# Kernel optimization log

Measured on AMD Instinct MI355X. Metric: run time of the kernel, lower is better.

## Reference

```python
import jax, jax.numpy as jnp
import numpy as np

N_GOAL, N_OBS, N_TASK = 16384, 65536, 8192
E1, E2 = 1048576, 1048576
B = 256            # graphs in batch
F, S = 128, 64     # dim_features, dim_state


def setup_inputs() -> dict:
    key = jax.random.key(0)
    ks = jax.random.split(key, 16)
    inp = {
        "x_goal": jax.random.normal(ks[0], (N_GOAL, F), jnp.float32),
        "x_obs": jax.random.normal(ks[1], (N_OBS, F), jnp.float32),
        "x_task": jax.random.normal(ks[2], (N_TASK, S), jnp.float32),
        "ei_go_src": jax.random.randint(ks[3], (E1,), 0, N_GOAL),
        "ei_go_dst": jax.random.randint(ks[4], (E1,), 0, N_OBS),
        "ei_ot_src": jax.random.randint(ks[5], (E2,), 0, N_OBS),
        "ei_ot_dst": jax.random.randint(ks[6], (E2,), 0, N_TASK),
        # contiguous graph assignment: 32 task nodes per graph
        "task_batch": jnp.arange(N_TASK) // (N_TASK // B),
        # GinStandardMLP (state_gin): Lin(F,S)-ReLU-Lin(S,S)-ReLU
        "W1": jax.random.normal(ks[7], (F, S), jnp.float32) * 0.05,
        "b1": jnp.zeros((S,), jnp.float32),
        "W2": jax.random.normal(ks[8], (S, S), jnp.float32) * 0.05,
        "b2": jnp.zeros((S,), jnp.float32),
        # GinUnactivatedMLP (action_gin): Lin(S,S)-ReLU-Lin(S,1)
        "W3": jax.random.normal(ks[9], (S, S), jnp.float32) * 0.05,
        "b3": jnp.zeros((S,), jnp.float32),
        "W4": jax.random.normal(ks[10], (S, 1), jnp.float32) * 0.05,
        "b4": jnp.zeros((1,), jnp.float32),
        # critic head: Lin(2,8)-ReLU-Lin(8,1)
        "Wc1": jax.random.normal(ks[11], (2, 8), jnp.float32) * 0.5,
        "bc1": jnp.zeros((8,), jnp.float32),
        "Wc2": jax.random.normal(ks[12], (8, 1), jnp.float32) * 0.5,
        "bc2": jnp.zeros((1,), jnp.float32),
    }
    return inp


def reference(x_goal, x_obs, x_task,
              ei_go_src, ei_go_dst, ei_ot_src, ei_ot_dst, task_batch,
              W1, b1, W2, b2, W3, b3, W4, b4, Wc1, bc1, Wc2, bc2):
    # --- state_gin: GINConv((goal, obs)), eps=0 ---
    agg1 = jax.ops.segment_sum(x_goal[ei_go_src], ei_go_dst, num_segments=N_OBS)
    h = x_obs + agg1                              # (1+eps)*x_dst + sum_j x_src
    h = jax.nn.relu(h @ W1 + b1)
    x1 = jax.nn.relu(h @ W2 + b2)                 # [N_OBS, S]

    # --- action_gin: GINConv((obs, task)), eps=0 ---
    agg2 = jax.ops.segment_sum(x1[ei_ot_src], ei_ot_dst, num_segments=N_TASK)
    g = x_task + agg2
    g = jax.nn.relu(g @ W3 + b3)
    x2 = g @ W4 + b4                              # [N_TASK, 1]

    # --- critic path: global max / mean pool over task nodes per graph ---
    max_pool = jax.ops.segment_max(x2, task_batch, num_segments=B)   # [B, 1]
    cnt = jax.ops.segment_sum(jnp.ones((N_TASK, 1), x2.dtype), task_batch, num_segments=B)
    mean_pool = jax.ops.segment_sum(x2, task_batch, num_segments=B) / cnt  # [B, 1]

    pooled = jnp.concatenate([max_pool.max(axis=1, keepdims=True),
                              mean_pool.mean(axis=1, keepdims=True)], axis=1)  # [B, 2]
    out = jax.nn.relu(pooled @ Wc1 + bc1) @ Wc2 + bc2                 # [B, 1]
    return out.squeeze(-1)                                            # [B]
```

## Files before the change

kernel.cpp:

```cpp
#include <hip/hip_runtime.h>
#include <hip/hip_bf16.h>


#define NB 512
#define BUCKET_CAP 2816

__global__ __launch_bounds__(256) void gemm_k128(
    const float* __restrict__ X, const float* __restrict__ W,
    float* __restrict__ out, int M)
{
    __shared__ float Ws[128 * 64];
    __shared__ float Xs[16 * 132];
    const int tid = threadIdx.x;
    for (int i = tid; i < 128 * 64 / 4; i += 256)
        ((float4*)Ws)[i] = ((const float4*)W)[i];
    const int row0 = blockIdx.x * 16;
    for (int i = tid; i < 16 * 32; i += 256) {
        int r = i >> 5, c4 = i & 31;
        float4 v = ((const float4*)(X + (size_t)(row0 + r) * 128))[c4];
        *((float4*)(Xs + r * 132 + c4 * 4)) = v;
    }
    __syncthreads();
    const int rl = tid >> 4;
    const int cg = (tid & 15) * 4;
    float a0 = 0.f, a1 = 0.f, a2 = 0.f, a3 = 0.f;
    const float* xr = Xs + rl * 132;
    #pragma unroll 8
    for (int k = 0; k < 128; ++k) {
        float xv = xr[k];
        float4 wv = *((const float4*)(Ws + k * 64 + cg));
        a0 = fmaf(xv, wv.x, a0);
        a1 = fmaf(xv, wv.y, a1);
        a2 = fmaf(xv, wv.z, a2);
        a3 = fmaf(xv, wv.w, a3);
    }
    float4 o; o.x = a0; o.y = a1; o.z = a2; o.w = a3;
    *((float4*)(out + (size_t)(row0 + rl) * 64 + cg)) = o;
}

template <int BSH>
__global__ __launch_bounds__(256) void bin_edges(
    const int* __restrict__ src, const int* __restrict__ dst,
    int* __restrict__ gcur, int2* __restrict__ pairs)
{
    __shared__ int hist[NB];
    __shared__ int cur[NB];
    const int tid = threadIdx.x;
    for (int i = tid; i < NB; i += 256) hist[i] = 0;
    __syncthreads();
    const int base = blockIdx.x * 4096;
    const int4* d4 = (const int4*)(dst + base);
    const int4* s4 = (const int4*)(src + base);
    int4 dv[4];
    #pragma unroll
    for (int k = 0; k < 4; ++k) {
        dv[k] = d4[k * 256 + tid];
        atomicAdd(&hist[dv[k].x >> BSH], 1);
        atomicAdd(&hist[dv[k].y >> BSH], 1);
        atomicAdd(&hist[dv[k].z >> BSH], 1);
        atomicAdd(&hist[dv[k].w >> BSH], 1);
    }
    __syncthreads();
    for (int i = tid; i < NB; i += 256)
        cur[i] = atomicAdd(&gcur[i], hist[i]);
    __syncthreads();
    #pragma unroll
    for (int k = 0; k < 4; ++k) {
        int4 sv = s4[k * 256 + tid];
        int d, s, b, p;
        d = dv[k].x; s = sv.x; b = d >> BSH; p = atomicAdd(&cur[b], 1);
        if (p < BUCKET_CAP) pairs[(size_t)b * BUCKET_CAP + p] = make_int2(d, s);
        d = dv[k].y; s = sv.y; b = d >> BSH; p = atomicAdd(&cur[b], 1);
        if (p < BUCKET_CAP) pairs[(size_t)b * BUCKET_CAP + p] = make_int2(d, s);
        d = dv[k].z; s = sv.z; b = d >> BSH; p = atomicAdd(&cur[b], 1);
        if (p < BUCKET_CAP) pairs[(size_t)b * BUCKET_CAP + p] = make_int2(d, s);
        d = dv[k].w; s = sv.w; b = d >> BSH; p = atomicAdd(&cur[b], 1);
        if (p < BUCKET_CAP) pairs[(size_t)b * BUCKET_CAP + p] = make_int2(d, s);
    }
}

template <int BSH, bool ADD_BASE>
__global__ __launch_bounds__(1024) void gather_sorted(
    const int2* __restrict__ pairs, const int* __restrict__ cnt,
    const float* __restrict__ table, float* __restrict__ outb)
{
    constexpr int ROWS = 1 << BSH;
    constexpr int ROWM = ROWS - 1;
    __shared__ int ssrc[BUCKET_CAP];
    __shared__ int offs[ROWS + 1];
    __shared__ int cur[ROWS];
    __shared__ int sc[ROWS];
    const int tid = threadIdx.x;
    const int b = blockIdx.x;

    for (int i = tid; i < ROWS; i += 1024) cur[i] = 0;
    __syncthreads();
    int n = cnt[b];
    if (n > BUCKET_CAP) n = BUCKET_CAP;
    const int2* bp = pairs + (size_t)b * BUCKET_CAP;

    for (int i = tid; i < n; i += 1024)
        atomicAdd(&cur[bp[i].x & ROWM], 1);
    __syncthreads();
    if (tid < ROWS) sc[tid] = cur[tid];
    __syncthreads();
    for (int off = 1; off < ROWS; off <<= 1) {
        int v = 0;
        if (tid < ROWS && tid >= off) v = sc[tid - off];
        __syncthreads();
        if (tid < ROWS) sc[tid] += v;
        __syncthreads();
    }
    if (tid < ROWS) {
        int ex = (tid == 0) ? 0 : sc[tid - 1];
        offs[tid] = ex;
        cur[tid] = ex;
        if (tid == ROWS - 1) offs[ROWS] = sc[tid];
    }
    __syncthreads();
    for (int i = tid; i < n; i += 1024) {
        int2 p = bp[i];
        int pos = atomicAdd(&cur[p.x & ROWM], 1);
        ssrc[pos] = p.y;
    }
    __syncthreads();
    const int wv = tid >> 6;
    const int lane = tid & 63;
    for (int r = wv; r < ROWS; r += 16) {
        int beg = offs[r], end = offs[r + 1];
        float a0 = 0.f, a1 = 0.f, a2 = 0.f, a3 = 0.f;
        int e = beg;
        for (; e + 4 <= end; e += 4) {
            int s0 = ssrc[e], s1 = ssrc[e + 1], s2 = ssrc[e + 2], s3 = ssrc[e + 3];
            a0 += table[(size_t)s0 * 64 + lane];
            a1 += table[(size_t)s1 * 64 + lane];
            a2 += table[(size_t)s2 * 64 + lane];
            a3 += table[(size_t)s3 * 64 + lane];
        }
        for (; e < end; ++e)
            a0 += table[(size_t)ssrc[e] * 64 + lane];
        float acc = (a0 + a1) + (a2 + a3);
        size_t gi = (((size_t)b << BSH) + r) * 64 + lane;
        if (ADD_BASE) acc += outb[gi];
        outb[gi] = acc;
    }
}

__global__ __launch_bounds__(256) void mlp_obs(
    const float* __restrict__ in, const float* __restrict__ b1,
    const float* __restrict__ W2, const float* __restrict__ b2,
    float* __restrict__ out, int M)
{
    __shared__ float Ws[64 * 64];
    __shared__ float Hs[16 * 68];
    const int tid = threadIdx.x;
    for (int i = tid; i < 64 * 64 / 4; i += 256)
        ((float4*)Ws)[i] = ((const float4*)W2)[i];
    const int row0 = blockIdx.x * 16;
    {
        int r = tid >> 4, c4 = tid & 15;
        float4 v = ((const float4*)(in + (size_t)(row0 + r) * 64))[c4];
        float4 bb = ((const float4*)b1)[c4];
        v.x = fmaxf(v.x + bb.x, 0.f);
        v.y = fmaxf(v.y + bb.y, 0.f);
        v.z = fmaxf(v.z + bb.z, 0.f);
        v.w = fmaxf(v.w + bb.w, 0.f);
        *((float4*)(Hs + r * 68 + c4 * 4)) = v;
    }
    __syncthreads();
    const int rl = tid >> 4, cg = (tid & 15) * 4;
    float4 bb2 = *((const float4*)(b2 + cg));
    float a0 = bb2.x, a1 = bb2.y, a2 = bb2.z, a3 = bb2.w;
    const float* hr = Hs + rl * 68;
    #pragma unroll 8
    for (int k = 0; k < 64; ++k) {
        float xv = hr[k];
        float4 wv = *((const float4*)(Ws + k * 64 + cg));
        a0 = fmaf(xv, wv.x, a0);
        a1 = fmaf(xv, wv.y, a1);
        a2 = fmaf(xv, wv.z, a2);
        a3 = fmaf(xv, wv.w, a3);
    }
    float4 o;
    o.x = fmaxf(a0, 0.f); o.y = fmaxf(a1, 0.f);
    o.z = fmaxf(a2, 0.f); o.w = fmaxf(a3, 0.f);
    *((float4*)(out + (size_t)(row0 + rl) * 64 + cg)) = o;
}

__global__ __launch_bounds__(512) void mlp_task_pool(
    const float* __restrict__ x_task, const float* __restrict__ acc2,
    const float* __restrict__ W3, const float* __restrict__ b3,
    const float* __restrict__ W4, const float* __restrict__ b4,
    const float* __restrict__ Wc1, const float* __restrict__ bc1,
    const float* __restrict__ Wc2, const float* __restrict__ bc2,
    float* __restrict__ out)
{
    __shared__ float Ws[64 * 64];
    __shared__ float Ts[32 * 68];
    __shared__ float xrow[32];
    const int tid = threadIdx.x;
    for (int i = tid; i < 64 * 64 / 4; i += 512)
        ((float4*)Ws)[i] = ((const float4*)W3)[i];
    const int row0 = blockIdx.x * 32;
    {
        int r = tid >> 4, c4 = tid & 15;
        size_t off = (size_t)(row0 + r) * 64;
        float4 v = ((const float4*)(x_task + off))[c4];
        float4 u = ((const float4*)(acc2 + off))[c4];
        v.x += u.x; v.y += u.y; v.z += u.z; v.w += u.w;
        *((float4*)(Ts + r * 68 + c4 * 4)) = v;
    }
    __syncthreads();
    const int rl = tid >> 4, cg = (tid & 15) * 4;
    float4 bb = *((const float4*)(b3 + cg));
    float a0 = bb.x, a1 = bb.y, a2 = bb.z, a3 = bb.w;
    const float* tr = Ts + rl * 68;
    #pragma unroll 8
    for (int k = 0; k < 64; ++k) {
        float xv = tr[k];
        float4 wv = *((const float4*)(Ws + k * 64 + cg));
        a0 = fmaf(xv, wv.x, a0);
        a1 = fmaf(xv, wv.y, a1);
        a2 = fmaf(xv, wv.z, a2);
        a3 = fmaf(xv, wv.w, a3);
    }
    float4 w4 = *((const float4*)(W4 + cg));
    float p = fmaxf(a0, 0.f) * w4.x + fmaxf(a1, 0.f) * w4.y
            + fmaxf(a2, 0.f) * w4.z + fmaxf(a3, 0.f) * w4.w;
    p += __shfl_xor(p, 1);
    p += __shfl_xor(p, 2);
    p += __shfl_xor(p, 4);
    p += __shfl_xor(p, 8);
    if ((tid & 15) == 0) xrow[rl] = p + b4[0];
    __syncthreads();
    if (tid == 0) {
        float mx = -1e30f, sm = 0.f;
        #pragma unroll
        for (int i = 0; i < 32; ++i) { float v = xrow[i]; mx = fmaxf(mx, v); sm += v; }
        float mn = sm * (1.f / 32.f);
        float o = bc2[0];
        #pragma unroll
        for (int j = 0; j < 8; ++j) {
            float t = fmaxf(mx * Wc1[j] + mn * Wc1[8 + j] + bc1[j], 0.f);
            o = fmaf(t, Wc2[j], o);
        }
        out[blockIdx.x] = o;
    }
}

extern "C" void kernel_launch(void* const* d_in, const int* in_sizes, int n_in,
                              void* d_out, int out_size, void* d_ws, size_t ws_size,
                              hipStream_t stream)
{
    const float* x_goal = (const float*)d_in[0];
    const float* x_obs  = (const float*)d_in[1];
    const float* x_task = (const float*)d_in[2];
    const int* go_src = (const int*)d_in[3];
    const int* go_dst = (const int*)d_in[4];
    const int* ot_src = (const int*)d_in[5];
    const int* ot_dst = (const int*)d_in[6];
    const float* W1  = (const float*)d_in[8];
    const float* b1  = (const float*)d_in[9];
    const float* W2  = (const float*)d_in[10];
    const float* b2  = (const float*)d_in[11];
    const float* W3  = (const float*)d_in[12];
    const float* b3  = (const float*)d_in[13];
    const float* W4  = (const float*)d_in[14];
    const float* b4  = (const float*)d_in[15];
    const float* Wc1 = (const float*)d_in[16];
    const float* bc1 = (const float*)d_in[17];
    const float* Wc2 = (const float*)d_in[18];
    const float* bc2 = (const float*)d_in[19];
    float* out = (float*)d_out;

    const int N_GOAL = 16384, N_OBS = 65536, N_TASK = 8192;
    const int E1 = in_sizes[3], E2 = in_sizes[5];

    char* w = (char*)d_ws;
    float* obs   = (float*)w;   w += (size_t)N_OBS * 64 * 4;
    float* xg1   = (float*)w;   w += (size_t)N_GOAL * 64 * 4;
    float* acc2  = (float*)w;   w += (size_t)N_TASK * 64 * 4;
    int2*  pairs = (int2*)w;    w += (size_t)NB * BUCKET_CAP * 8;
    int*   gcur1 = (int*)w;     w += NB * 4;
    int*   gcur2 = (int*)w;     w += NB * 4;

    hipMemsetAsync(gcur1, 0, 2 * NB * 4, stream);

    bin_edges<7><<<E1 / 4096, 256, 0, stream>>>(go_src, go_dst, gcur1, pairs);
    gemm_k128<<<N_GOAL / 16, 256, 0, stream>>>(x_goal, W1, xg1, N_GOAL);
    gemm_k128<<<N_OBS / 16, 256, 0, stream>>>(x_obs, W1, obs, N_OBS);
    gather_sorted<7, true><<<NB, 1024, 0, stream>>>(pairs, gcur1, xg1, obs);
    mlp_obs<<<N_OBS / 16, 256, 0, stream>>>(obs, b1, W2, b2, obs, N_OBS);

    bin_edges<4><<<E2 / 4096, 256, 0, stream>>>(ot_src, ot_dst, gcur2, pairs);
    gather_sorted<4, false><<<NB, 1024, 0, stream>>>(pairs, gcur2, obs, acc2);
    mlp_task_pool<<<N_TASK / 32, 512, 0, stream>>>(x_task, acc2, W3, b3, W4, b4,
                                                   Wc1, bc1, Wc2, bc2, out);
}
```

Measured before the change: 270.7 us.

## Fuse gathers with MLP layers and pack edge pairs into single ints

Edge pairs are packed into one 32-bit int (local row in the high bits, source index in the low 17 bits), which halves bucket traffic. The obs gather is fused with bias, ReLU and the W2 layer, and the task gather is fused with the W3 and W4 layers. This removes the separate mlp_obs and mlp_task_pool passes and their intermediate round trips through global memory. Pooling moves to a tiny single-block kernel, and the second binning now runs early into its own buffer. The fused per-wave 64x64 matvec from shared memory may use compute less efficiently than the old tiled GEMM.

```diff
diff --git a/kernel.cpp b/kernel.cpp
--- a/kernel.cpp
+++ b/kernel.cpp
@@ -41,8 +41,9 @@
 template <int BSH>
 __global__ __launch_bounds__(256) void bin_edges(
     const int* __restrict__ src, const int* __restrict__ dst,
-    int* __restrict__ gcur, int2* __restrict__ pairs)
-{
+    int* __restrict__ gcur, int* __restrict__ pairs)
+{
+    constexpr int ROWM = (1 << BSH) - 1;
     __shared__ int hist[NB];
     __shared__ int cur[NB];
     const int tid = threadIdx.x;
@@ -69,38 +70,41 @@
         int4 sv = s4[k * 256 + tid];
         int d, s, b, p;
         d = dv[k].x; s = sv.x; b = d >> BSH; p = atomicAdd(&cur[b], 1);
-        if (p < BUCKET_CAP) pairs[(size_t)b * BUCKET_CAP + p] = make_int2(d, s);
+        if (p < BUCKET_CAP) pairs[(size_t)b * BUCKET_CAP + p] = ((d & ROWM) << 17) | s;
         d = dv[k].y; s = sv.y; b = d >> BSH; p = atomicAdd(&cur[b], 1);
-        if (p < BUCKET_CAP) pairs[(size_t)b * BUCKET_CAP + p] = make_int2(d, s);
+        if (p < BUCKET_CAP) pairs[(size_t)b * BUCKET_CAP + p] = ((d & ROWM) << 17) | s;
         d = dv[k].z; s = sv.z; b = d >> BSH; p = atomicAdd(&cur[b], 1);
-        if (p < BUCKET_CAP) pairs[(size_t)b * BUCKET_CAP + p] = make_int2(d, s);
+        if (p < BUCKET_CAP) pairs[(size_t)b * BUCKET_CAP + p] = ((d & ROWM) << 17) | s;
         d = dv[k].w; s = sv.w; b = d >> BSH; p = atomicAdd(&cur[b], 1);
-        if (p < BUCKET_CAP) pairs[(size_t)b * BUCKET_CAP + p] = make_int2(d, s);
-    }
-}
-
-template <int BSH, bool ADD_BASE>
-__global__ __launch_bounds__(1024) void gather_sorted(
-    const int2* __restrict__ pairs, const int* __restrict__ cnt,
-    const float* __restrict__ table, float* __restrict__ outb)
-{
-    constexpr int ROWS = 1 << BSH;
-    constexpr int ROWM = ROWS - 1;
+        if (p < BUCKET_CAP) pairs[(size_t)b * BUCKET_CAP + p] = ((d & ROWM) << 17) | s;
+    }
+}
+
+__global__ __launch_bounds__(1024) void gather_mlp_obs(
+    const int* __restrict__ pairs, const int* __restrict__ cnt,
+    const float* __restrict__ xg1, const float* __restrict__ obs,
+    const float* __restrict__ b1, const float* __restrict__ W2,
+    const float* __restrict__ b2, float* __restrict__ x1)
+{
+    constexpr int ROWS = 128;
     __shared__ int ssrc[BUCKET_CAP];
     __shared__ int offs[ROWS + 1];
     __shared__ int cur[ROWS];
     __shared__ int sc[ROWS];
+    __shared__ float W2s[64 * 64];
+    __shared__ float hb[16 * 64];
     const int tid = threadIdx.x;
     const int b = blockIdx.x;
 
-    for (int i = tid; i < ROWS; i += 1024) cur[i] = 0;
+    ((float4*)W2s)[tid] = ((const float4*)W2)[tid];
+    if (tid < ROWS) cur[tid] = 0;
     __syncthreads();
     int n = cnt[b];
     if (n > BUCKET_CAP) n = BUCKET_CAP;
-    const int2* bp = pairs + (size_t)b * BUCKET_CAP;
+    const int* bp = pairs + (size_t)b * BUCKET_CAP;
 
     for (int i = tid; i < n; i += 1024)
-        atomicAdd(&cur[bp[i].x & ROWM], 1);
+        atomicAdd(&cur[bp[i] >> 17], 1);
     __syncthreads();
     if (tid < ROWS) sc[tid] = cur[tid];
     __syncthreads();
@@ -119,133 +123,149 @@
     }
     __syncthreads();
     for (int i = tid; i < n; i += 1024) {
-        int2 p = bp[i];
-        int pos = atomicAdd(&cur[p.x & ROWM], 1);
-        ssrc[pos] = p.y;
+        int p = bp[i];
+        int pos = atomicAdd(&cur[p >> 17], 1);
+        ssrc[pos] = p & 0x1FFFF;
     }
     __syncthreads();
     const int wv = tid >> 6;
     const int lane = tid & 63;
+    const float bb1 = b1[lane];
+    const float bb2 = b2[lane];
+    float* hp = hb + wv * 64;
     for (int r = wv; r < ROWS; r += 16) {
         int beg = offs[r], end = offs[r + 1];
         float a0 = 0.f, a1 = 0.f, a2 = 0.f, a3 = 0.f;
         int e = beg;
         for (; e + 4 <= end; e += 4) {
             int s0 = ssrc[e], s1 = ssrc[e + 1], s2 = ssrc[e + 2], s3 = ssrc[e + 3];
-            a0 += table[(size_t)s0 * 64 + lane];
-            a1 += table[(size_t)s1 * 64 + lane];
-            a2 += table[(size_t)s2 * 64 + lane];
-            a3 += table[(size_t)s3 * 64 + lane];
+            a0 += xg1[(size_t)s0 * 64 + lane];
+            a1 += xg1[(size_t)s1 * 64 + lane];
+            a2 += xg1[(size_t)s2 * 64 + lane];
+            a3 += xg1[(size_t)s3 * 64 + lane];
         }
         for (; e < end; ++e)
-            a0 += table[(size_t)ssrc[e] * 64 + lane];
-        float acc = (a0 + a1) + (a2 + a3);
-        size_t gi = (((size_t)b << BSH) + r) * 64 + lane;
-        if (ADD_BASE) acc += outb[gi];
-        outb[gi] = acc;
-    }
-}
-
-__global__ __launch_bounds__(256) void mlp_obs(
-    const float* __restrict__ in, const float* __restrict__ b1,
-    const float* __restrict__ W2, const float* __restrict__ b2,
-    float* __restrict__ out, int M)
-{
-    __shared__ float Ws[64 * 64];
-    __shared__ float Hs[16 * 68];
-    const int tid = threadIdx.x;
-    for (int i = tid; i < 64 * 64 / 4; i += 256)
-        ((float4*)Ws)[i] = ((const float4*)W2)[i];
-    const int row0 = blockIdx.x * 16;
-    {
-        int r = tid >> 4, c4 = tid & 15;
-        float4 v = ((const float4*)(in + (size_t)(row0 + r) * 64))[c4];
-        float4 bb = ((const float4*)b1)[c4];
-        v.x = fmaxf(v.x + bb.x, 0.f);
-        v.y = fmaxf(v.y + bb.y, 0.f);
-        v.z = fmaxf(v.z + bb.z, 0.f);
-        v.w = fmaxf(v.w + bb.w, 0.f);
-        *((float4*)(Hs + r * 68 + c4 * 4)) = v;
-    }
-    __syncthreads();
-    const int rl = tid >> 4, cg = (tid & 15) * 4;
-    float4 bb2 = *((const float4*)(b2 + cg));
-    float a0 = bb2.x, a1 = bb2.y, a2 = bb2.z, a3 = bb2.w;
-    const float* hr = Hs + rl * 68;
-    #pragma unroll 8
-    for (int k = 0; k < 64; ++k) {
-        float xv = hr[k];
-        float4 wv = *((const float4*)(Ws + k * 64 + cg));
-        a0 = fmaf(xv, wv.x, a0);
-        a1 = fmaf(xv, wv.y, a1);
-        a2 = fmaf(xv, wv.z, a2);
-        a3 = fmaf(xv, wv.w, a3);
-    }
-    float4 o;
-    o.x = fmaxf(a0, 0.f); o.y = fmaxf(a1, 0.f);
-    o.z = fmaxf(a2, 0.f); o.w = fmaxf(a3, 0.f);
-    *((float4*)(out + (size_t)(row0 + rl) * 64 + cg)) = o;
-}
-
-__global__ __launch_bounds__(512) void mlp_task_pool(
-    const float* __restrict__ x_task, const float* __restrict__ acc2,
+            a0 += xg1[(size_t)ssrc[e] * 64 + lane];
+        size_t gi = (((size_t)b * ROWS) + r) * 64 + lane;
+        float acc = (a0 + a1) + (a2 + a3) + obs[gi];
+        hp[lane] = fmaxf(acc + bb1, 0.f);
+        float a = bb2;
+        #pragma unroll 16
+        for (int k = 0; k < 64; ++k)
+            a = fmaf(hp[k], W2s[k * 64 + lane], a);
+        x1[gi] = fmaxf(a, 0.f);
+    }
+}
+
+__global__ __launch_bounds__(1024) void gather_mlp_task(
+    const int* __restrict__ pairs, const int* __restrict__ cnt,
+    const float* __restrict__ x1, const float* __restrict__ x_task,
     const float* __restrict__ W3, const float* __restrict__ b3,
     const float* __restrict__ W4, const float* __restrict__ b4,
-    const float* __restrict__ Wc1, const float* __restrict__ bc1,
-    const float* __restrict__ Wc2, const float* __restrict__ bc2,
-    float* __restrict__ out)
-{
-    __shared__ float Ws[64 * 64];
-    __shared__ float Ts[32 * 68];
-    __shared__ float xrow[32];
+    float* __restrict__ x2)
+{
+    constexpr int ROWS = 16;
+    __shared__ int ssrc[BUCKET_CAP];
+    __shared__ int offs[ROWS + 1];
+    __shared__ int cur[ROWS];
+    __shared__ int sc[ROWS];
+    __shared__ float W3s[64 * 64];
+    __shared__ float hb[16 * 64];
     const int tid = threadIdx.x;
-    for (int i = tid; i < 64 * 64 / 4; i += 512)
-        ((float4*)Ws)[i] = ((const float4*)W3)[i];
-    const int row0 = blockIdx.x * 32;
-    {
-        int r = tid >> 4, c4 = tid & 15;
-        size_t off = (size_t)(row0 + r) * 64;
-        float4 v = ((const float4*)(x_task + off))[c4];
-        float4 u = ((const float4*)(acc2 + off))[c4];
-        v.x += u.x; v.y += u.y; v.z += u.z; v.w += u.w;
-        *((float4*)(Ts + r * 68 + c4 * 4)) = v;
-    }
-    __syncthreads();
-    const int rl = tid >> 4, cg = (tid & 15) * 4;
-    float4 bb = *((const float4*)(b3 + cg));
-    float a0 = bb.x, a1 = bb.y, a2 = bb.z, a3 = bb.w;
-    const float* tr = Ts + rl * 68;
-    #pragma unroll 8
-    for (int k = 0; k < 64; ++k) {
-        float xv = tr[k];
-        float4 wv = *((const float4*)(Ws + k * 64 + cg));
-        a0 = fmaf(xv, wv.x, a0);
-        a1 = fmaf(xv, wv.y, a1);
-        a2 = fmaf(xv, wv.z, a2);
-        a3 = fmaf(xv, wv.w, a3);
-    }
-    float4 w4 = *((const float4*)(W4 + cg));
-    float p = fmaxf(a0, 0.f) * w4.x + fmaxf(a1, 0.f) * w4.y
-            + fmaxf(a2, 0.f) * w4.z + fmaxf(a3, 0.f) * w4.w;
+    const int b = blockIdx.x;
+
+    ((float4*)W3s)[tid] = ((const float4*)W3)[tid];
+    if (tid < ROWS) cur[tid] = 0;
+    __syncthreads();
+    int n = cnt[b];
+    if (n > BUCKET_CAP) n = BUCKET_CAP;
+    const int* bp = pairs + (size_t)b * BUCKET_CAP;
+
+    for (int i = tid; i < n; i += 1024)
+        atomicAdd(&cur[bp[i] >> 17], 1);
+    __syncthreads();
+    if (tid < ROWS) sc[tid] = cur[tid];
+    __syncthreads();
+    for (int off = 1; off < ROWS; off <<= 1) {
+        int v = 0;
+        if (tid < ROWS && tid >= off) v = sc[tid - off];
+        __syncthreads();
+        if (tid < ROWS) sc[tid] += v;
+        __syncthreads();
+    }
+    if (tid < ROWS) {
+        int ex = (tid == 0) ? 0 : sc[tid - 1];
+        offs[tid] = ex;
+        cur[tid] = ex;
+        if (tid == ROWS - 1) offs[ROWS] = sc[tid];
+    }
+    __syncthreads();
+    for (int i = tid; i < n; i += 1024) {
+        int p = bp[i];
+        int pos = atomicAdd(&cur[p >> 17], 1);
+        ssrc[pos] = p & 0x1FFFF;
+    }
+    __syncthreads();
+
+    const int wv = tid >> 6;
+    const int lane = tid & 63;
+    const int r = wv;
+    const int row = b * ROWS + r;
+    int beg = offs[r], end = offs[r + 1];
+    float a0 = 0.f, a1 = 0.f, a2 = 0.f, a3 = 0.f;
+    float a4 = 0.f, a5 = 0.f, a6 = 0.f, a7 = 0.f;
+    int e = beg;
+    for (; e + 8 <= end; e += 8) {
+        int s0 = ssrc[e],     s1 = ssrc[e + 1], s2 = ssrc[e + 2], s3 = ssrc[e + 3];
+        int s4 = ssrc[e + 4], s5 = ssrc[e + 5], s6 = ssrc[e + 6], s7 = ssrc[e + 7];
+        a0 += x1[(size_t)s0 * 64 + lane];
+        a1 += x1[(size_t)s1 * 64 + lane];
+        a2 += x1[(size_t)s2 * 64 + lane];
+        a3 += x1[(size_t)s3 * 64 + lane];
+        a4 += x1[(size_t)s4 * 64 + lane];
+        a5 += x1[(size_t)s5 * 64 + lane];
+        a6 += x1[(size_t)s6 * 64 + lane];
+        a7 += x1[(size_t)s7 * 64 + lane];
+    }
+    for (; e < end; ++e)
+        a0 += x1[(size_t)ssrc[e] * 64 + lane];
+    float t = ((a0 + a1) + (a2 + a3)) + ((a4 + a5) + (a6 + a7))
+            + x_task[(size_t)row * 64 + lane];
+    float* hp = hb + wv * 64;
+    hp[lane] = t;
+    float a = b3[lane];
+    #pragma unroll 16
+    for (int k = 0; k < 64; ++k)
+        a = fmaf(hp[k], W3s[k * 64 + lane], a);
+    float p = fmaxf(a, 0.f) * W4[lane];
     p += __shfl_xor(p, 1);
     p += __shfl_xor(p, 2);
     p += __shfl_xor(p, 4);
     p += __shfl_xor(p, 8);
-    if ((tid & 15) == 0) xrow[rl] = p + b4[0];
-    __syncthreads();
-    if (tid == 0) {
-        float mx = -1e30f, sm = 0.f;
-        #pragma unroll
-        for (int i = 0; i < 32; ++i) { float v = xrow[i]; mx = fmaxf(mx, v); sm += v; }
-        float mn = sm * (1.f / 32.f);
-        float o = bc2[0];
-        #pragma unroll
-        for (int j = 0; j < 8; ++j) {
-            float t = fmaxf(mx * Wc1[j] + mn * Wc1[8 + j] + bc1[j], 0.f);
-            o = fmaf(t, Wc2[j], o);
-        }
-        out[blockIdx.x] = o;
-    }
+    p += __shfl_xor(p, 16);
+    p += __shfl_xor(p, 32);
+    if (lane == 0)
+        x2[row] = p + b4[0];
+}
+
+__global__ __launch_bounds__(256) void pool_critic(
+    const float* __restrict__ x2, const float* __restrict__ Wc1,
+    const float* __restrict__ bc1, const float* __restrict__ Wc2,
+    const float* __restrict__ bc2, float* __restrict__ out)
+{
+    int b = threadIdx.x;
+    const float* p = x2 + b * 32;
+    float mx = -1e30f, sm = 0.f;
+    #pragma unroll
+    for (int i = 0; i < 32; ++i) { float v = p[i]; mx = fmaxf(mx, v); sm += v; }
+    float mn = sm * (1.f / 32.f);
+    float o = bc2[0];
+    #pragma unroll
+    for (int j = 0; j < 8; ++j) {
+        float t = fmaxf(mx * Wc1[j] + mn * Wc1[8 + j] + bc1[j], 0.f);
+        o = fmaf(t, Wc2[j], o);
+    }
+    out[b] = o;
 }
 
 extern "C" void kernel_launch(void* const* d_in, const int* in_sizes, int n_in,
@@ -277,23 +297,22 @@
     const int E1 = in_sizes[3], E2 = in_sizes[5];
 
     char* w = (char*)d_ws;
-    float* obs   = (float*)w;   w += (size_t)N_OBS * 64 * 4;
-    float* xg1   = (float*)w;   w += (size_t)N_GOAL * 64 * 4;
-    float* acc2  = (float*)w;   w += (size_t)N_TASK * 64 * 4;
-    int2*  pairs = (int2*)w;    w += (size_t)NB * BUCKET_CAP * 8;
-    int*   gcur1 = (int*)w;     w += NB * 4;
-    int*   gcur2 = (int*)w;     w += NB * 4;
+    float* obs    = (float*)w;  w += (size_t)N_OBS * 64 * 4;
+    float* x1     = (float*)w;  w += (size_t)N_OBS * 64 * 4;
+    float* xg1    = (float*)w;  w += (size_t)N_GOAL * 64 * 4;
+    float* x2     = (float*)w;  w += (size_t)N_TASK * 4;
+    int*   pairs1 = (int*)w;    w += (size_t)NB * BUCKET_CAP * 4;
+    int*   pairs2 = (int*)w;    w += (size_t)NB * BUCKET_CAP * 4;
+    int*   gcur1  = (int*)w;    w += NB * 4;
+    int*   gcur2  = (int*)w;    w += NB * 4;
 
     hipMemsetAsync(gcur1, 0, 2 * NB * 4, stream);
 
-    bin_edges<7><<<E1 / 4096, 256, 0, stream>>>(go_src, go_dst, gcur1, pairs);
+    bin_edges<7><<<E1 / 4096, 256, 0, stream>>>(go_src, go_dst, gcur1, pairs1);
+    bin_edges<4><<<E2 / 4096, 256, 0, stream>>>(ot_src, ot_dst, gcur2, pairs2);
     gemm_k128<<<N_GOAL / 16, 256, 0, stream>>>(x_goal, W1, xg1, N_GOAL);
     gemm_k128<<<N_OBS / 16, 256, 0, stream>>>(x_obs, W1, obs, N_OBS);
-    gather_sorted<7, true><<<NB, 1024, 0, stream>>>(pairs, gcur1, xg1, obs);
-    mlp_obs<<<N_OBS / 16, 256, 0, stream>>>(obs, b1, W2, b2, obs, N_OBS);
-
-    bin_edges<4><<<E2 / 4096, 256, 0, stream>>>(ot_src, ot_dst, gcur2, pairs);
-    gather_sorted<4, false><<<NB, 1024, 0, stream>>>(pairs, gcur2, obs, acc2);
-    mlp_task_pool<<<N_TASK / 32, 512, 0, stream>>>(x_task, acc2, W3, b3, W4, b4,
-                                                   Wc1, bc1, Wc2, bc2, out);
-}
+    gather_mlp_obs<<<NB, 1024, 0, stream>>>(pairs1, gcur1, xg1, obs, b1, W2, b2, x1);
+    gather_mlp_task<<<NB, 1024, 0, stream>>>(pairs2, gcur2, x1, x_task, W3, b3, W4, b4, x2);
+    pool_critic<<<1, 256, 0, stream>>>(x2, Wc1, bc1, Wc2, bc2, out);
+}
```

New measurement: 264.2 us. 2.4% less time.
